# Optimization experiments

Hardware: AMD Instinct MI355X
Metric: run time of the kernel (lower is better)

The kernel has to match this reference:

```python
import jax, jax.numpy as jnp
import numpy as np

DN = ('NCHW', 'OIHW', 'NCHW')

def conv(x, w, b=None, pad='SAME'):
    y = jax.lax.conv_general_dilated(x, w, (1, 1), pad, dimension_numbers=DN)
    if b is not None:
        y = y + b[None, :, None, None]
    return y

def prelu(x, a):
    return jnp.where(x >= 0, x, a * x)

def ca_layer(x, w_a, w_b):
    # global avg pool -> 1x1 conv -> relu -> 1x1 conv -> sigmoid -> gate
    g = jnp.mean(x, axis=(2, 3), keepdims=True)          # [B,C,1,1]
    g = jax.nn.relu(conv(g, w_a))
    g = jax.nn.sigmoid(conv(g, w_b))
    return x * g

def head(x, w, b, ca_a, ca_b):
    y = conv(x, w, b)                                    # [B,4,H,W]
    y = ca_layer(y, ca_a, ca_b)
    return jax.nn.softmax(y, axis=1)                     # Softmax2d = softmax over C

def box_kernel(k):
    return jnp.full((1, 1, k, k), 1.0 / (k * k), dtype=jnp.float32)

def multiscale_blur(x):
    # SAME-padded uniform box filters of sizes 1,5,15,25 on [B,1,H,W]
    return [x if k == 1 else conv(x, box_kernel(k)) for k in (1, 5, 15, 25)]

def weighted_combine(h, blurs):
    # h: [B,4,H,W] softmax weights; blurs: list of 4 [B,1,H,W]
    return sum(h[:, i:i+1] * blurs[i] for i in range(4))

def setup_inputs() -> dict:
    key = jax.random.key(0)
    ks = jax.random.split(key, 32)
    B, H, W = 8, 512, 512
    s = 0.05
    inp = {
        'x':  jax.random.normal(ks[0], (B, 1, H, W), jnp.float32),
        'w1': jax.random.normal(ks[1], (32, 1, 3, 3), jnp.float32) * s,
        'b1': jnp.zeros((32,), jnp.float32),
        'a1': jnp.float32(0.25),
        'w2': jax.random.normal(ks[2], (64, 32, 3, 3), jnp.float32) * s,
        'b2': jnp.zeros((64,), jnp.float32),
        'a2': jnp.float32(0.25),
        'w3': jax.random.normal(ks[3], (32, 64, 3, 3), jnp.float32) * s,
        'b3': jnp.zeros((32,), jnp.float32),
        'a3': jnp.float32(0.25),
    }
    for i, kk in zip((1, 2, 3), (4, 8, 12)):
        inp[f'hw{i}'] = jax.random.normal(ks[kk], (4, 32, 3, 3), jnp.float32) * s
        inp[f'hb{i}'] = jnp.zeros((4,), jnp.float32)
        inp[f'ca{i}a'] = jax.random.normal(ks[kk + 1], (4, 4, 1, 1), jnp.float32) * s
        inp[f'ca{i}b'] = jax.random.normal(ks[kk + 2], (4, 4, 1, 1), jnp.float32) * s
    return inp

def reference(x, w1, b1, a1, w2, b2, a2, w3, b3, a3,
              hw1, hb1, ca1a, ca1b, hw2, hb2, ca2a, ca2b, hw3, hb3, ca3a, ca3b):
    body = prelu(conv(x, w1, b1), a1)
    body = prelu(conv(body, w2, b2), a2)
    body = prelu(conv(body, w3, b3), a3)            # [B,32,H,W]
    h1 = head(body, hw1, hb1, ca1a, ca1b)
    h2 = head(body, hw2, hb2, ca2a, ca2b)
    h3 = head(body, hw3, hb3, ca3a, ca3b)
    out1 = weighted_combine(h1, multiscale_blur(x))
    out2 = weighted_combine(h2, multiscale_blur(out1))
    out3 = weighted_combine(h3, multiscale_blur(out2))
    return out3
```

## Files before the change

kernel.cpp:

```cpp
#include <hip/hip_runtime.h>

#define HH 512
#define WW 512
#define NB 8
#define HWSZ (HH * WW)
#define PW 516
#define PROWS 514

typedef float f32x4 __attribute__((ext_vector_type(4)));
typedef float f32x16 __attribute__((ext_vector_type(16)));
typedef short bf16x8 __attribute__((ext_vector_type(8)));

__device__ __forceinline__ unsigned short f2bf(float f) {
  union { float f; unsigned u; } v; v.f = f;
  unsigned r = v.u + 0x7FFFu + ((v.u >> 16) & 1u);
  return (unsigned short)(r >> 16);
}
__device__ __forceinline__ float bf2f(unsigned u16) {
  union { unsigned u; float f; } v; v.u = u16 << 16;
  return v.f;
}

__device__ __forceinline__ void gload16(const uint4* g, uint4* l) {
  __builtin_amdgcn_global_load_lds((__attribute__((address_space(1))) void*)g,
                                   (__attribute__((address_space(3))) void*)l, 16, 0, 0);
}

#define PS1 ((size_t)PROWS * PW * 32)
#define PS2 ((size_t)PROWS * PW * 64)
#define NZ1 (2 * 4 * PW * 8 + 512 * 4 * 16)
#define NZ2 (2 * 8 * PW * 8 + 512 * 8 * 16)

__device__ __forceinline__ void zp(unsigned short* buf, int NCH, int i) {
  int rowShorts = NCH * PW * 8;
  if (i < 2 * rowShorts) {
    size_t r = (i < rowShorts) ? 0 : 513;
    int j = i % rowShorts;
    buf[r * rowShorts + j] = 0;
    return;
  }
  i -= 2 * rowShorts;
  int perRow = NCH * 16;
  int r = 1 + i / perRow;
  int j = i % perRow;
  int ch = j >> 4;
  int c = (j & 8) ? 513 : 0;
  int e = j & 7;
  buf[(((size_t)r * NCH + ch) * PW + c) * 8 + e] = 0;
}

__global__ __launch_bounds__(256) void k_prep(const float* __restrict__ w2,
                                              const float* __restrict__ w3,
                                              const float* __restrict__ h0,
                                              const float* __restrict__ h1,
                                              const float* __restrict__ h2,
                                              unsigned short* __restrict__ wp2,
                                              unsigned short* __restrict__ wp3,
                                              unsigned short* __restrict__ wph,
                                              unsigned short* __restrict__ t1,
                                              unsigned short* __restrict__ t2,
                                              float* __restrict__ S) {
  int i = blockIdx.x * 256 + threadIdx.x;
  const int N1 = 9 * 64 * 32;
  const int N2 = N1 + 9 * 32 * 64;
  const int N3 = N2 + 9 * 16 * 32;
  const int N4 = N3 + 4 * NZ1;
  const int N5 = N4 + 4 * NZ2;
  const int N6 = N5 + 128;
  if (i < N1) {
    int j8 = i & 7;
    int lane = (i >> 3) & 63;
    int mt = (i >> 9) & 1;
    int ks = (i >> 10) & 1;
    int tap = i >> 11;
    int l31 = lane & 31, h16 = lane >> 5;
    int oc = mt * 32 + l31;
    int ic = ks * 16 + h16 * 8 + j8;
    wp2[i] = f2bf(w2[(oc * 32 + ic) * 9 + tap]);
  } else if (i < N2) {
    int j = i - N1;
    int j8 = j & 7;
    int lane = (j >> 3) & 63;
    int ks = (j >> 9) & 3;
    int tap = j >> 11;
    int l31 = lane & 31, h16 = lane >> 5;
    int ic = ks * 16 + h16 * 8 + j8;
    wp3[j] = f2bf(w3[(l31 * 64 + ic) * 9 + tap]);
  } else if (i < N3) {
    int j = i - N2;
    int ic = j & 31, t = j >> 5, oc = t & 15, k = t >> 4;
    float v = 0.f;
    if (oc < 12) {
      const float* w = oc < 4 ? h0 : (oc < 8 ? h1 : h2);
      v = w[((oc & 3) * 32 + ic) * 9 + k];
    }
    wph[j] = f2bf(v);
  } else if (i < N4) {
    int j = i - N3;
    zp(t1 + (size_t)(j / NZ1) * PS1, 4, j % NZ1);
  } else if (i < N5) {
    int j = i - N4;
    zp(t2 + (size_t)(j / NZ2) * PS2, 8, j % NZ2);
  } else if (i < N6) {
    S[i - N5] = 0.f;
  }
}

__global__ __launch_bounds__(256) void k_conv1(const float* __restrict__ x,
                                               const float* __restrict__ w,
                                               const float* __restrict__ bias,
                                               const float* __restrict__ a_ptr,
                                               unsigned short* __restrict__ out) {
  const float* xp = x + (size_t)blockIdx.z * HWSZ;
  uint4* out4 = (uint4*)(out + (size_t)blockIdx.z * PS1);
  int pix = blockIdx.x * 256 + threadIdx.x;
  int h = pix >> 9, wc = pix & 511;
  float t[9];
#pragma unroll
  for (int dh = 0; dh < 3; dh++)
#pragma unroll
    for (int dw = 0; dw < 3; dw++) {
      int hh = h + dh - 1, ww = wc + dw - 1;
      t[dh * 3 + dw] =
          (hh >= 0 && hh < HH && ww >= 0 && ww < WW) ? xp[hh * WW + ww] : 0.f;
    }
  float a = a_ptr[0];
  unsigned pk[16];
#pragma unroll
  for (int oc = 0; oc < 32; oc++) {
    float s = bias[oc];
#pragma unroll
    for (int k = 0; k < 9; k++) s = fmaf(w[oc * 9 + k], t[k], s);
    s = s >= 0.f ? s : a * s;
    unsigned short b = f2bf(s);
    if (oc & 1)
      pk[oc >> 1] |= ((unsigned)b) << 16;
    else
      pk[oc >> 1] = b;
  }
#pragma unroll
  for (int q = 0; q < 4; q++)
    out4[((size_t)(h + 1) * 4 + q) * PW + (wc + 1)] = *(uint4*)&pk[q * 4];
}

__global__ __launch_bounds__(256, 2) void k_convm2(const unsigned short* __restrict__ in,
                                                   const unsigned short* __restrict__ wp,
                                                   const float* __restrict__ bias,
                                                   const float* __restrict__ a_ptr,
                                                   unsigned short* __restrict__ out) {
  __shared__ __align__(16) short ring[10 * 4 * 68 * 8];
  __shared__ __align__(16) short wlds[9 * 2 * 2 * 64 * 8];
  const int tid = threadIdx.x, lane = tid & 63, wid = tid >> 6;
  const int l31 = lane & 31, h16 = lane >> 5;
  const int c0 = blockIdx.x * 64;
  const int R0 = blockIdx.y * 32;
  const uint4* in4 = (const uint4*)(in + (size_t)blockIdx.z * PS1);
  unsigned short* outz = out + (size_t)blockIdx.z * PS2;
  uint4* ring4 = (uint4*)ring;
  uint4* wl4 = (uint4*)wlds;
  const uint4* wp4 = (const uint4*)wp;

  for (int sg = wid; sg < 36; sg += 4)
    gload16(wp4 + sg * 64 + lane, wl4 + sg * 64);

  auto load_rows = [&](int rfirst, int nrows) {
    int nseg = nrows * 4;
    for (int sg = wid; sg < nseg; sg += 4) {
      int rr = rfirst + (sg >> 2);
      int ch = sg & 3;
      const uint4* src = in4 + (size_t)(rr * 4 + ch) * PW + c0;
      uint4* dst = ring4 + ((rr % 10) * 4 + ch) * 68;
      gload16(src + lane, dst);
      gload16(src + 4 + lane, dst + 4);
    }
  };

  const float alpha = a_ptr[0];
  load_rows(R0, 6);

  for (int k = 0; k < 8; ++k) {
    const int rb = R0 + 4 * k;
    __syncthreads();
    if (k < 7) load_rows(rb + 6, 4);

    f32x16 acc[2][2];
#pragma unroll
    for (int nt = 0; nt < 2; nt++)
#pragma unroll
      for (int mt = 0; mt < 2; mt++)
#pragma unroll
        for (int j = 0; j < 16; j++) acc[nt][mt][j] = 0.f;

#pragma unroll
    for (int dh = 0; dh < 3; dh++) {
      bf16x8 af[3][2][2];
#pragma unroll
      for (int dw = 0; dw < 3; dw++)
#pragma unroll
        for (int ks = 0; ks < 2; ks++)
#pragma unroll
          for (int mt = 0; mt < 2; mt++)
            af[dw][ks][mt] = *(const bf16x8*)(
                wlds + ((((size_t)((dh * 3 + dw) * 2 + ks) * 2 + mt) * 64 + lane) * 8));
      const short* lrow = ring + (size_t)(((rb + wid + dh) % 10) * 4) * 68 * 8;
#pragma unroll
      for (int dw = 0; dw < 3; dw++) {
        const int pl0 = l31 + dw, pl1 = 32 + l31 + dw;
#pragma unroll
        for (int ks = 0; ks < 2; ks++) {
          const int blk = ks * 2 + h16;
          bf16x8 b0 = *(const bf16x8*)(lrow + (blk * 68 + pl0) * 8);
          bf16x8 b1 = *(const bf16x8*)(lrow + (blk * 68 + pl1) * 8);
#pragma unroll
          for (int mt = 0; mt < 2; mt++)
            acc[0][mt] = __builtin_amdgcn_mfma_f32_32x32x16_bf16(af[dw][ks][mt],
                                                                 b0, acc[0][mt], 0, 0, 0);
#pragma unroll
          for (int mt = 0; mt < 2; mt++)
            acc[1][mt] = __builtin_amdgcn_mfma_f32_32x32x16_bf16(af[dw][ks][mt],
                                                                 b1, acc[1][mt], 0, 0, 0);
        }
      }
    }

    const int orow = rb + wid + 1;
    uint2* o2 = (uint2*)outz;
#pragma unroll
    for (int nt = 0; nt < 2; nt++) {
      const int ocol = c0 + nt * 32 + l31 + 1;
#pragma unroll
      for (int mt = 0; mt < 2; mt++)
#pragma unroll
        for (int g = 0; g < 4; g++) {
          int oc0 = mt * 32 + g * 8 + h16 * 4;
          f32x4 bv = *(const f32x4*)(bias + oc0);
          float v[4];
#pragma unroll
          for (int j = 0; j < 4; j++) {
            float s = acc[nt][mt][g * 4 + j] + bv[j];
            v[j] = s >= 0.f ? s : alpha * s;
          }
          uint2 pk;
          pk.x = (unsigned)f2bf(v[0]) | ((unsigned)f2bf(v[1]) << 16);
          pk.y = (unsigned)f2bf(v[2]) | ((unsigned)f2bf(v[3]) << 16);
          size_t idx16 = ((size_t)orow * 8 + (mt * 4 + g)) * PW + ocol;
          o2[idx16 * 2 + h16] = pk;
        }
    }
  }
}

__global__ __launch_bounds__(256, 2) void k_convm3(const unsigned short* __restrict__ in,
                                                   const unsigned short* __restrict__ wp,
                                                   const float* __restrict__ bias,
                                                   const float* __restrict__ a_ptr,
                                                   unsigned short* __restrict__ out) {
  __shared__ __align__(16) short ring[8 * 8 * 36 * 8];
  __shared__ __align__(16) short wlds[9 * 4 * 64 * 8];
  const int tid = threadIdx.x, lane = tid & 63, wid = tid >> 6;
  const int l31 = lane & 31, h16 = lane >> 5;
  const int c0 = blockIdx.x * 32;
  const int R0 = blockIdx.y * 32;
  const uint4* in4 = (const uint4*)(in + (size_t)blockIdx.z * PS2);
  unsigned short* outz = out + (size_t)blockIdx.z * PS1;
  uint4* ring4 = (uint4*)ring;
  uint4* wl4 = (uint4*)wlds;
  const uint4* wp4 = (const uint4*)wp;

  for (int sg = wid; sg < 36; sg += 4)
    gload16(wp4 + sg * 64 + lane, wl4 + sg * 64);

  auto load_rows = [&](int rfirst, int nrows) {
    int nseg = nrows * 8;
    for (int sg = wid; sg < nseg; sg += 4) {
      int rr = rfirst + (sg >> 3);
      int ch = sg & 7;
      const uint4* src = in4 + (size_t)(rr * 8 + ch) * PW + c0;
      uint4* dst = ring4 + ((rr & 7) * 8 + ch) * 36;
      if (lane < 36) gload16(src + lane, dst);
    }
  };

  const float alpha = a_ptr[0];
  load_rows(R0, 6);

  for (int k = 0; k < 8; ++k) {
    const int rb = R0 + 4 * k;
    __syncthreads();
    if (k < 7) load_rows(rb + 6, 2);

    f32x16 acc;
#pragma unroll
    for (int j = 0; j < 16; j++) acc[j] = 0.f;

#pragma unroll
    for (int dh = 0; dh < 3; dh++) {
      bf16x8 af[3][4];
#pragma unroll
      for (int dw = 0; dw < 3; dw++)
#pragma unroll
        for (int ks = 0; ks < 4; ks++)
          af[dw][ks] = *(const bf16x8*)(
              wlds + (((size_t)((dh * 3 + dw) * 4 + ks) * 64 + lane) * 8));
      const short* lrow = ring + (size_t)(((rb + wid + dh) & 7) * 8) * 36 * 8;
#pragma unroll
      for (int dw = 0; dw < 3; dw++) {
        const int pl = l31 + dw;
#pragma unroll
        for (int ks = 0; ks < 4; ks++) {
          const int blk = ks * 2 + h16;
          bf16x8 b = *(const bf16x8*)(lrow + (blk * 36 + pl) * 8);
          acc = __builtin_amdgcn_mfma_f32_32x32x16_bf16(af[dw][ks], b, acc, 0, 0, 0);
        }
      }
    }

    const int orow = rb + wid + 1;
    const int ocol = c0 + l31 + 1;
    uint2* o2 = (uint2*)outz;
#pragma unroll
    for (int g = 0; g < 4; g++) {
      int oc0 = g * 8 + h16 * 4;
      f32x4 bv = *(const f32x4*)(bias + oc0);
      float v[4];
#pragma unroll
      for (int j = 0; j < 4; j++) {
        float s = acc[g * 4 + j] + bv[j];
        v[j] = s >= 0.f ? s : alpha * s;
      }
      uint2 pk;
      pk.x = (unsigned)f2bf(v[0]) | ((unsigned)f2bf(v[1]) << 16);
      pk.y = (unsigned)f2bf(v[2]) | ((unsigned)f2bf(v[3]) << 16);
      size_t idx16 = ((size_t)orow * 4 + g) * PW + ocol;
      o2[idx16 * 2 + h16] = pk;
    }
    __syncthreads();
    if (k < 7) load_rows(rb + 8, 2);
  }
}

__global__ __launch_bounds__(256, 2) void k_headm(const unsigned short* __restrict__ in,
                                                  const unsigned short* __restrict__ wp,
                                                  const float* __restrict__ hb0,
                                                  const float* __restrict__ hb1,
                                                  const float* __restrict__ hb2,
                                                  unsigned short* __restrict__ pre,
                                                  float* __restrict__ S) {
  __shared__ __align__(16) short lds[8 * 4 * 68 * 8];
  __shared__ float part[4][4][4];
  const int tid = threadIdx.x, lane = tid & 63, wid = tid >> 6;
  const int l15 = lane & 15, q = lane >> 4;
  const int c0 = blockIdx.x * 64;
  const int R0 = blockIdx.y * 32;
  const uint4* in4 = (const uint4*)(in + (size_t)blockIdx.z * PS1);
  float* Sz = S + blockIdx.z * 16;
  uint4* lds4 = (uint4*)lds;

  bf16x8 af[9];
#pragma unroll
  for (int k9 = 0; k9 < 9; k9++)
    af[k9] = *(const bf16x8*)(wp + (size_t)(k9 * 16 + l15) * 32 + q * 8);

  float bs[4];
#pragma unroll
  for (int r = 0; r < 4; r++) {
    int oc = q * 4 + r;
    bs[r] = oc < 4 ? hb0[oc] : (oc < 8 ? hb1[oc - 4] : (oc < 12 ? hb2[oc - 8] : 0.f));
  }
  unsigned short* prehq = pre + ((size_t)(q * 4 + blockIdx.z) * HWSZ) * 4;

  auto load_rows = [&](int rfirst, int nrows) {
    int nseg = nrows * 4;
    for (int sg = wid; sg < nseg; sg += 4) {
      int rr = rfirst + (sg >> 2);
      int ch = sg & 3;
      const uint4* src = in4 + (size_t)(rr * 4 + ch) * PW + c0;
      uint4* dst = lds4 + ((rr & 7) * 4 + ch) * 68;
      gload16(src + lane, dst);
      gload16(src + 4 + lane, dst + 4);
    }
  };

  load_rows(R0, 6);
  float csum[4] = {0.f, 0.f, 0.f, 0.f};

  for (int k = 0; k < 8; ++k) {
    const int rb = R0 + 4 * k;
    __syncthreads();
    if (k < 7) load_rows(rb + 6, 2);

    f32x4 acc[4];
#pragma unroll
    for (int nt = 0; nt < 4; nt++)
#pragma unroll
      for (int j = 0; j < 4; j++) acc[nt][j] = 0.f;

#pragma unroll
    for (int dh = 0; dh < 3; dh++) {
      const short* lrow = lds + (size_t)(((rb + wid + dh) & 7) * 4) * 68 * 8;
#pragma unroll
      for (int dw = 0; dw < 3; dw++) {
        bf16x8 a = af[dh * 3 + dw];
#pragma unroll
        for (int nt = 0; nt < 4; nt++) {
          int pl = nt * 16 + l15 + dw;
          bf16x8 b = *(const bf16x8*)(lrow + (q * 68 + pl) * 8);
          acc[nt] = __builtin_amdgcn_mfma_f32_16x16x32_bf16(a, b, acc[nt], 0, 0, 0);
        }
      }
    }

    const int orow = rb + wid;
#pragma unroll
    for (int nt = 0; nt < 4; nt++) {
      int pix = orow * 512 + c0 + nt * 16 + l15;
      float v[4];
#pragma unroll
      for (int r = 0; r < 4; r++) {
        v[r] = acc[nt][r] + bs[r];
        csum[r] += v[r];
      }
      uint2 pk;
      pk.x = (unsigned)f2bf(v[0]) | ((unsigned)f2bf(v[1]) << 16);
      pk.y = (unsigned)f2bf(v[2]) | ((unsigned)f2bf(v[3]) << 16);
      *(uint2*)(prehq + (size_t)pix * 4) = pk;
    }
    __syncthreads();
    if (k < 7) load_rows(rb + 8, 2);
  }

#pragma unroll
  for (int d = 1; d < 16; d <<= 1)
#pragma unroll
    for (int r = 0; r < 4; r++) csum[r] += __shfl_xor(csum[r], d, 64);
  if (l15 == 0)
#pragma unroll
    for (int r = 0; r < 4; r++) part[wid][q][r] = csum[r];
  __syncthreads();
  if (tid < 12) {
    int oc = tid;
    float s = part[0][oc >> 2][oc & 3] + part[1][oc >> 2][oc & 3] +
              part[2][oc >> 2][oc & 3] + part[3][oc >> 2][oc & 3];
    atomicAdd(&Sz[oc], s);
  }
}

#define BT 32
#define RAD 12
#define SRCT (BT + 2 * RAD)
__global__ __launch_bounds__(256) void k_blurcombine(const float* __restrict__ src,
                                                     const unsigned short* __restrict__ preh,
                                                     const float* __restrict__ S4,
                                                     const float* __restrict__ wa,
                                                     const float* __restrict__ wb,
                                                     float* __restrict__ dst) {
  __shared__ float tile[SRCT][SRCT];
  __shared__ float hs[3][SRCT][BT];
  __shared__ float g[4];
  const float* srcz = src + (size_t)blockIdx.z * HWSZ;
  const unsigned short* prez = preh + (size_t)blockIdx.z * HWSZ * 4;
  const float* S4z = S4 + blockIdx.z * 16;
  float* dstz = dst + (size_t)blockIdx.z * HWSZ;
  int h0 = blockIdx.y * BT - RAD, w0 = blockIdx.x * BT - RAD;
  if (threadIdx.x < 4) {
    int o = threadIdx.x;
    float m[4], ga[4];
#pragma unroll
    for (int c = 0; c < 4; c++) m[c] = S4z[c] * (1.0f / (float)HWSZ);
#pragma unroll
    for (int c = 0; c < 4; c++) {
      float s = 0.f;
#pragma unroll
      for (int j = 0; j < 4; j++) s = fmaf(wa[c * 4 + j], m[j], s);
      ga[c] = fmaxf(s, 0.f);
    }
    float s2 = 0.f;
#pragma unroll
    for (int c = 0; c < 4; c++) s2 = fmaf(wb[o * 4 + c], ga[c], s2);
    g[o] = 1.f / (1.f + expf(-s2));
  }
  for (int idx = threadIdx.x; idx < SRCT * SRCT; idx += 256) {
    int r = idx / SRCT, c = idx % SRCT;
    int hh = h0 + r, ww = w0 + c;
    float v = 0.f;
    if (hh >= 0 && hh < HH && ww >= 0 && ww < WW) v = srcz[hh * WW + ww];
    tile[r][c] = v;
  }
  __syncthreads();
  for (int idx = threadIdx.x; idx < SRCT * BT; idx += 256) {
    int r = idx / BT, j = idx % BT;
    int cc = j + RAD;
    float s5 = 0.f;
#pragma unroll
    for (int d = -2; d <= 2; d++) s5 += tile[r][cc + d];
    float s15 = s5;
#pragma unroll
    for (int d = 3; d <= 7; d++) s15 += tile[r][cc + d] + tile[r][cc - d];
    float s25 = s15;
#pragma unroll
    for (int d = 8; d <= 12; d++) s25 += tile[r][cc + d] + tile[r][cc - d];
    hs[0][r][j] = s5;
    hs[1][r][j] = s15;
    hs[2][r][j] = s25;
  }
  __syncthreads();
  for (int p = threadIdx.x; p < BT * BT; p += 256) {
    int i = p / BT, j = p % BT;
    int rr = i + RAD;
    float b1 = 0.f;
#pragma unroll
    for (int d = -2; d <= 2; d++) b1 += hs[0][rr + d][j];
    float b2 = 0.f;
#pragma unroll
    for (int d = -7; d <= 7; d++) b2 += hs[1][rr + d][j];
    float b3 = 0.f;
#pragma unroll
    for (int d = -12; d <= 12; d++) b3 += hs[2][rr + d][j];
    b1 *= (1.f / 25.f);
    b2 *= (1.f / 225.f);
    b3 *= (1.f / 625.f);
    float b0 = tile[rr][j + RAD];
    int y = blockIdx.y * BT + i, x = blockIdx.x * BT + j;
    int pix = y * WW + x;
    uint2 pk = *(const uint2*)(prez + (size_t)pix * 4);
    float v[4];
    v[0] = bf2f(pk.x & 0xffffu) * g[0];
    v[1] = bf2f(pk.x >> 16) * g[1];
    v[2] = bf2f(pk.y & 0xffffu) * g[2];
    v[3] = bf2f(pk.y >> 16) * g[3];
    float mx = fmaxf(fmaxf(v[0], v[1]), fmaxf(v[2], v[3]));
    float e0 = expf(v[0] - mx), e1 = expf(v[1] - mx), e2 = expf(v[2] - mx),
          e3 = expf(v[3] - mx);
    float inv = 1.f / (e0 + e1 + e2 + e3);
    dstz[pix] = (e0 * b0 + e1 * b1 + e2 * b2 + e3 * b3) * inv;
  }
}

extern "C" void kernel_launch(void* const* d_in, const int* in_sizes, int n_in,
                              void* d_out, int out_size, void* d_ws, size_t ws_size,
                              hipStream_t stream) {
  const float* x = (const float*)d_in[0];
  const float* w1 = (const float*)d_in[1];
  const float* b1 = (const float*)d_in[2];
  const float* a1 = (const float*)d_in[3];
  const float* w2 = (const float*)d_in[4];
  const float* b2 = (const float*)d_in[5];
  const float* a2 = (const float*)d_in[6];
  const float* w3 = (const float*)d_in[7];
  const float* b3 = (const float*)d_in[8];
  const float* a3 = (const float*)d_in[9];
  const float* hw[3] = {(const float*)d_in[10], (const float*)d_in[14], (const float*)d_in[18]};
  const float* hb[3] = {(const float*)d_in[11], (const float*)d_in[15], (const float*)d_in[19]};
  const float* caa[3] = {(const float*)d_in[12], (const float*)d_in[16], (const float*)d_in[20]};
  const float* cab[3] = {(const float*)d_in[13], (const float*)d_in[17], (const float*)d_in[21]};

  char* base = (char*)d_ws;
  size_t off = 0;
  auto alloc = [&](size_t bytes) {
    char* p = base + off;
    off = (off + bytes + 63) & ~(size_t)63;
    return p;
  };
  unsigned short* t1 = (unsigned short*)alloc(4 * PS1 * 2);
  unsigned short* t2 = (unsigned short*)alloc(4 * PS2 * 2);
  unsigned short* pre = (unsigned short*)alloc(16 * (size_t)HWSZ * 4 * 2);
  unsigned short* wp2 = (unsigned short*)alloc(9 * 64 * 32 * 2);
  unsigned short* wp3 = (unsigned short*)alloc(9 * 64 * 32 * 2);
  unsigned short* wph = (unsigned short*)alloc(9 * 16 * 32 * 2);
  float* out1 = (float*)alloc(4 * (size_t)HWSZ * 4);
  float* out2 = (float*)alloc(4 * (size_t)HWSZ * 4);
  float* S = (float*)alloc(8 * 16 * 4);

  dim3 blk(256);
  {
    int total = 9 * 64 * 32 + 9 * 32 * 64 + 9 * 16 * 32 + 4 * NZ1 + 4 * NZ2 + 128;
    k_prep<<<(total + 255) / 256, blk, 0, stream>>>(w2, w3, hw[0], hw[1], hw[2], wp2,
                                                    wp3, wph, t1, t2, S);
  }

  dim3 gc1(1024, 1, 4);
  dim3 gconv(8, 16, 4);
  dim3 gconv3(16, 16, 4);
  dim3 gbc(WW / BT, HH / BT, 4);
  const size_t preplane = (size_t)HWSZ * 4;
  for (int g = 0; g < 2; g++) {
    const float* xg = x + (size_t)g * 4 * HWSZ;
    float* Sg = S + g * 64;
    float* outg = (float*)d_out + (size_t)g * 4 * HWSZ;
    k_conv1<<<gc1, blk, 0, stream>>>(xg, w1, b1, a1, t1);
    k_convm2<<<gconv, blk, 0, stream>>>(t1, wp2, b2, a2, t2);
    k_convm3<<<gconv3, blk, 0, stream>>>(t2, wp3, b3, a3, t1);
    k_headm<<<gconv, blk, 0, stream>>>(t1, wph, hb[0], hb[1], hb[2], pre, Sg);
    k_blurcombine<<<gbc, blk, 0, stream>>>(xg, pre + 0 * 4 * preplane, Sg + 0, caa[0], cab[0], out1);
    k_blurcombine<<<gbc, blk, 0, stream>>>(out1, pre + 1 * 4 * preplane, Sg + 4, caa[1], cab[1], out2);
    k_blurcombine<<<gbc, blk, 0, stream>>>(out2, pre + 2 * 4 * preplane, Sg + 8, caa[2], cab[2], outg);
  }
}
```

Measured before the change: 468.6 us.

## Split conv3 input channels across two wave groups with LDS reduction

The conv3 kernel now launches 512 threads per block, and the two groups of four waves each take half of the 64 input channels. Partial accumulators are summed through a shared-memory buffer before the bias, PReLU and bf16 store. Weights are kept in registers loaded straight from global memory instead of being staged in LDS. This is meant to raise wave-level parallelism and free LDS. In exchange it adds an LDS reduction step and more register use, which puts the launch_bounds occupancy target of 6 at risk.

After: 765.6 us. +63.4%, slower.

```diff
diff --git a/kernel.cpp b/kernel.cpp
--- a/kernel.cpp
+++ b/kernel.cpp
@@ -250,29 +250,34 @@
   }
 }
 
-__global__ __launch_bounds__(256, 2) void k_convm3(const unsigned short* __restrict__ in,
+__global__ __launch_bounds__(512, 6) void k_convm3(const unsigned short* __restrict__ in,
                                                    const unsigned short* __restrict__ wp,
                                                    const float* __restrict__ bias,
                                                    const float* __restrict__ a_ptr,
                                                    unsigned short* __restrict__ out) {
   __shared__ __align__(16) short ring[8 * 8 * 36 * 8];
-  __shared__ __align__(16) short wlds[9 * 4 * 64 * 8];
+  __shared__ __align__(16) float red[4 * 4 * 64 * 4];
   const int tid = threadIdx.x, lane = tid & 63, wid = tid >> 6;
   const int l31 = lane & 31, h16 = lane >> 5;
+  const int rw = wid & 3;
+  const int ih = wid >> 2;
   const int c0 = blockIdx.x * 32;
   const int R0 = blockIdx.y * 32;
   const uint4* in4 = (const uint4*)(in + (size_t)blockIdx.z * PS2);
   unsigned short* outz = out + (size_t)blockIdx.z * PS1;
   uint4* ring4 = (uint4*)ring;
-  uint4* wl4 = (uint4*)wlds;
-  const uint4* wp4 = (const uint4*)wp;
-
-  for (int sg = wid; sg < 36; sg += 4)
-    gload16(wp4 + sg * 64 + lane, wl4 + sg * 64);
+  f32x4* red4 = (f32x4*)red;
+
+  bf16x8 af[9][2];
+#pragma unroll
+  for (int t = 0; t < 9; t++)
+#pragma unroll
+    for (int kk = 0; kk < 2; kk++)
+      af[t][kk] = *(const bf16x8*)(wp + ((size_t)(t * 4 + ih * 2 + kk) * 64 + lane) * 8);
 
   auto load_rows = [&](int rfirst, int nrows) {
     int nseg = nrows * 8;
-    for (int sg = wid; sg < nseg; sg += 4) {
+    for (int sg = wid; sg < nseg; sg += 8) {
       int rr = rfirst + (sg >> 3);
       int ch = sg & 7;
       const uint4* src = in4 + (size_t)(rr * 8 + ch) * PW + c0;
@@ -295,47 +300,52 @@
 
 #pragma unroll
     for (int dh = 0; dh < 3; dh++) {
-      bf16x8 af[3][4];
-#pragma unroll
-      for (int dw = 0; dw < 3; dw++)
-#pragma unroll
-        for (int ks = 0; ks < 4; ks++)
-          af[dw][ks] = *(const bf16x8*)(
-              wlds + (((size_t)((dh * 3 + dw) * 4 + ks) * 64 + lane) * 8));
-      const short* lrow = ring + (size_t)(((rb + wid + dh) & 7) * 8) * 36 * 8;
+      const short* lrow = ring + (size_t)(((rb + rw + dh) & 7) * 8) * 36 * 8;
 #pragma unroll
       for (int dw = 0; dw < 3; dw++) {
         const int pl = l31 + dw;
 #pragma unroll
-        for (int ks = 0; ks < 4; ks++) {
-          const int blk = ks * 2 + h16;
+        for (int kk = 0; kk < 2; kk++) {
+          const int blk = (ih * 2 + kk) * 2 + h16;
           bf16x8 b = *(const bf16x8*)(lrow + (blk * 36 + pl) * 8);
-          acc = __builtin_amdgcn_mfma_f32_32x32x16_bf16(af[dw][ks], b, acc, 0, 0, 0);
+          acc = __builtin_amdgcn_mfma_f32_32x32x16_bf16(af[dh * 3 + dw][kk], b, acc,
+                                                        0, 0, 0);
         }
       }
     }
 
-    const int orow = rb + wid + 1;
-    const int ocol = c0 + l31 + 1;
-    uint2* o2 = (uint2*)outz;
-#pragma unroll
-    for (int g = 0; g < 4; g++) {
-      int oc0 = g * 8 + h16 * 4;
-      f32x4 bv = *(const f32x4*)(bias + oc0);
-      float v[4];
-#pragma unroll
-      for (int j = 0; j < 4; j++) {
-        float s = acc[g * 4 + j] + bv[j];
-        v[j] = s >= 0.f ? s : alpha * s;
+    if (ih == 1) {
+#pragma unroll
+      for (int g = 0; g < 4; g++) {
+        f32x4 v = {acc[g * 4 + 0], acc[g * 4 + 1], acc[g * 4 + 2], acc[g * 4 + 3]};
+        red4[(rw * 4 + g) * 64 + lane] = v;
       }
-      uint2 pk;
-      pk.x = (unsigned)f2bf(v[0]) | ((unsigned)f2bf(v[1]) << 16);
-      pk.y = (unsigned)f2bf(v[2]) | ((unsigned)f2bf(v[3]) << 16);
-      size_t idx16 = ((size_t)orow * 4 + g) * PW + ocol;
-      o2[idx16 * 2 + h16] = pk;
     }
     __syncthreads();
     if (k < 7) load_rows(rb + 8, 2);
+
+    if (ih == 0) {
+      const int orow = rb + rw + 1;
+      const int ocol = c0 + l31 + 1;
+      uint2* o2 = (uint2*)outz;
+#pragma unroll
+      for (int g = 0; g < 4; g++) {
+        f32x4 p = red4[(rw * 4 + g) * 64 + lane];
+        int oc0 = g * 8 + h16 * 4;
+        f32x4 bv = *(const f32x4*)(bias + oc0);
+        float v[4];
+#pragma unroll
+        for (int j = 0; j < 4; j++) {
+          float s = acc[g * 4 + j] + p[j] + bv[j];
+          v[j] = s >= 0.f ? s : alpha * s;
+        }
+        uint2 pk;
+        pk.x = (unsigned)f2bf(v[0]) | ((unsigned)f2bf(v[1]) << 16);
+        pk.y = (unsigned)f2bf(v[2]) | ((unsigned)f2bf(v[3]) << 16);
+        size_t idx16 = ((size_t)orow * 4 + g) * PW + ocol;
+        o2[idx16 * 2 + h16] = pk;
+      }
+    }
   }
 }
 
@@ -589,7 +599,7 @@
     float* outg = (float*)d_out + (size_t)g * 4 * HWSZ;
     k_conv1<<<gc1, blk, 0, stream>>>(xg, w1, b1, a1, t1);
     k_convm2<<<gconv, blk, 0, stream>>>(t1, wp2, b2, a2, t2);
-    k_convm3<<<gconv3, blk, 0, stream>>>(t2, wp3, b3, a3, t1);
+    k_convm3<<<gconv3, dim3(512), 0, stream>>>(t2, wp3, b3, a3, t1);
     k_headm<<<gconv, blk, 0, stream>>>(t1, wph, hb[0], hb[1], hb[2], pre, Sg);
     k_blurcombine<<<gbc, blk, 0, stream>>>(xg, pre + 0 * 4 * preplane, Sg + 0, caa[0], cab[0], out1);
     k_blurcombine<<<gbc, blk, 0, stream>>>(out1, pre + 1 * 4 * preplane, Sg + 4, caa[1], cab[1], out2);
```
